# Kernel tuning notes

Measured on AMD Instinct MI355X. Metric: run time of the kernel, lower is better.

The kernel has to match this reference:

```python
import jax, jax.numpy as jnp
import numpy as np

# Grid constants from init_kwargs: output_shape = [1, 10, 200, 176, 64]
D, H, W, C = 10, 200, 176, 64
N_VOX = 30000


def _conv_block(x, w, scale, bias, stride, pad):
    # x: [N,C,D,H,W]; w: [O,I,kd,kh,kw]; ZeroPad3d then valid Conv3d,
    # then fused (inference) BatchNorm3d + ReLU.
    x = jnp.pad(x, ((0, 0), (0, 0), (pad[0], pad[0]), (pad[1], pad[1]), (pad[2], pad[2])))
    x = jax.lax.conv_general_dilated(
        x, w, window_strides=stride, padding='VALID',
        dimension_numbers=('NCDHW', 'OIDHW', 'NCDHW'))
    s = scale[None, :, None, None, None]
    b = bias[None, :, None, None, None]
    return jax.nn.relu(x * s + b)


def setup_inputs() -> dict:
    key = jax.random.key(0)
    kf, kd, kh, kw, k1, k2, k3, ks = jax.random.split(key, 8)
    voxel_features = jax.random.normal(kf, (N_VOX, C), dtype=jnp.float32)
    # coors columns: (batch_idx, d, h, w) each in range
    b_idx = jnp.zeros((N_VOX,), dtype=jnp.int32)  # batch_size = 1
    d_idx = jax.random.randint(kd, (N_VOX,), 0, D, dtype=jnp.int32)
    h_idx = jax.random.randint(kh, (N_VOX,), 0, H, dtype=jnp.int32)
    w_idx = jax.random.randint(kw, (N_VOX,), 0, W, dtype=jnp.int32)
    coors = jnp.stack([b_idx, d_idx, h_idx, w_idx], axis=1)
    fan = 1.0 / np.sqrt(C * 27)
    W1 = jax.random.normal(k1, (64, C, 3, 3, 3), dtype=jnp.float32) * fan
    W2 = jax.random.normal(k2, (64, 64, 3, 3, 3), dtype=jnp.float32) * fan
    W3 = jax.random.normal(k3, (64, 64, 3, 3, 3), dtype=jnp.float32) * fan
    ks1, ks2, ks3 = jax.random.split(ks, 3)
    scale1 = jax.random.uniform(ks1, (64,), dtype=jnp.float32, minval=0.5, maxval=1.5)
    scale2 = jax.random.uniform(ks2, (64,), dtype=jnp.float32, minval=0.5, maxval=1.5)
    scale3 = jax.random.uniform(ks3, (64,), dtype=jnp.float32, minval=0.5, maxval=1.5)
    bias1 = jax.random.normal(jax.random.fold_in(ks1, 1), (64,), dtype=jnp.float32) * 0.1
    bias2 = jax.random.normal(jax.random.fold_in(ks2, 1), (64,), dtype=jnp.float32) * 0.1
    bias3 = jax.random.normal(jax.random.fold_in(ks3, 1), (64,), dtype=jnp.float32) * 0.1
    return {
        'voxel_features': voxel_features, 'coors': coors, 'batch_size': 1,
        'W1': W1, 'scale1': scale1, 'bias1': bias1,
        'W2': W2, 'scale2': scale2, 'bias2': bias2,
        'W3': W3, 'scale3': scale3, 'bias3': bias3,
    }


def reference(voxel_features, coors, batch_size,
              W1, scale1, bias1, W2, scale2, bias2, W3, scale3, bias3):
    # scatter_nd: sparse voxel features -> dense [B, D, H, W, C]
    dense = jnp.zeros((batch_size, D, H, W, C), dtype=voxel_features.dtype)
    dense = dense.at[coors[:, 0], coors[:, 1], coors[:, 2], coors[:, 3]].set(voxel_features)
    x = dense.transpose(0, 4, 1, 2, 3)  # [B, C, D, H, W]
    # middle_conv: Pad(1)+Conv3d s=(2,1,1); Pad(0,1,1)+Conv3d s=1; Pad(1)+Conv3d s=(2,1,1)
    x = _conv_block(x, W1, scale1, bias1, (2, 1, 1), (1, 1, 1))   # D: 10 -> 5
    x = _conv_block(x, W2, scale2, bias2, (1, 1, 1), (0, 1, 1))   # D: 5 -> 3
    x = _conv_block(x, W3, scale3, bias3, (2, 1, 1), (1, 1, 1))   # D: 3 -> 2
    N, Cc, Dd, Hh, Ww = x.shape
    return x.reshape(N, Cc * Dd, Hh, Ww)  # [B, 128, H, W]
```

## Files before the change

### kernel.cpp

```cpp
#include <hip/hip_runtime.h>
#include <cstddef>

#define HH 200
#define WW 176
#define HP 202
#define WP 178
#define D_IN 10
#define D1 5
#define D2 3
#define D3 2
#define SLICE ((size_t)HP * WP * 64)

#define LA_SZ 51200
#define LB0   102400
#define LB_SZ 24576
#define LDS_TOTAL 151552

typedef _Float16 h8 __attribute__((ext_vector_type(8)));
typedef float f4 __attribute__((ext_vector_type(4)));

__device__ __forceinline__ void gl_lds16(const void* g, void* l) {
    __builtin_amdgcn_global_load_lds(
        (const __attribute__((address_space(1))) void*)g,
        (__attribute__((address_space(3))) void*)l, 16, 0, 0);
}

__global__ __launch_bounds__(256) void prep_k(const float* __restrict__ W1,
                                              const float* __restrict__ W2,
                                              const float* __restrict__ W3,
                                              _Float16* __restrict__ wdst,
                                              _Float16* __restrict__ A2,
                                              _Float16* __restrict__ A3,
                                              const int* __restrict__ coors,
                                              int* __restrict__ winner, int nvox) {
    const int b = blockIdx.x;
    if (b < 8) {
        _Float16* base = (b < D1) ? (A2 + (size_t)b * SLICE) : (A3 + (size_t)(b - D1) * SLICE);
        const h8 z = {};
        for (int t = threadIdx.x; t < 6080; t += 256) {
            size_t off;
            if (t < 2848) {
                int r = t / 1424, c = t - r * 1424;
                off = (size_t)(r ? (HP - 1) : 0) * WP * 64 + (size_t)c * 8;
            } else {
                int u = t - 2848;
                int c = u / 1616, v = u - c * 1616;
                int hr = v >> 3, o = v & 7;
                off = ((size_t)hr * WP + (c ? (WP - 1) : 0)) * 64 + (size_t)o * 8;
            }
            *(h8*)(base + off) = z;
        }
    } else if (b < 8 + 1296) {
        int idx = (b - 8) * 256 + threadIdx.x;
        if (idx < 3 * 27 * 64 * 64) {
            int set = idx / 110592;
            int r = idx - set * 110592;
            const float* src = set == 0 ? W1 : (set == 1 ? W2 : W3);
            int ci = r & 63;
            int co = (r >> 6) & 63;
            int tap = r >> 12;
            int s = ci >> 3, j = ci & 7;
            wdst[set * 110592 + tap * 4096 + co * 64 + (((s ^ (co & 7)) << 3) | j)] =
                (_Float16)src[(co * 64 + ci) * 27 + tap];
        }
    } else {
        int v = (b - 1304) * 256 + threadIdx.x;
        if (v < nvox) {
            int d = coors[v * 4 + 1], h = coors[v * 4 + 2], w = coors[v * 4 + 3];
            atomicMax(&winner[(d * HH + h) * WW + w], v + 1);
        }
    }
}

__global__ __launch_bounds__(256) void scatter_k(const float* __restrict__ feat,
                                                 const int* __restrict__ coors,
                                                 const int* __restrict__ winner,
                                                 _Float16* __restrict__ A, int nvox) {
    int v = blockIdx.x * 4 + (threadIdx.x >> 6);
    int ci = threadIdx.x & 63;
    if (v >= nvox) return;
    int d = coors[v * 4 + 1], h = coors[v * 4 + 2], w = coors[v * 4 + 3];
    if (winner[(d * HH + h) * WW + w] != v + 1) return;
    int P = w + 1;
    int swz = (((ci >> 3) ^ (P & 7)) << 3) | (ci & 7);
    A[(size_t)d * SLICE + ((size_t)(h + 1) * WP + P) * 64 + swz] = (_Float16)feat[v * 64 + ci];
}

template <int FINAL>
__global__ __launch_bounds__(512, 2) void conv_mfma_k(
    const _Float16* __restrict__ in, void* __restrict__ outp,
    const _Float16* __restrict__ wt,
    const float* __restrict__ scale, const float* __restrict__ bias,
    int inD, int strideD, int padD) {
    extern __shared__ char smem[];

    const int lane = threadIdx.x & 63;
    const int wave = threadIdx.x >> 6;
    const int l16 = lane & 15;
    const int quad = lane >> 4;
    const int h0 = blockIdx.y * 8;
    const int wb = blockIdx.x * 48;
    const int d = blockIdx.z;

    int kd_lo = padD - d * strideD; if (kd_lo < 0) kd_lo = 0;
    int kd_hi = inD - 1 - d * strideD + padD; if (kd_hi > 2) kd_hi = 2;
    const int P = 3 * (kd_hi - kd_lo + 1);

    auto stage = [&](int p, int par) {
        const int kd = kd_lo + p / 3;
        const int kh = p - 3 * (p / 3);
        const int zd = d * strideD + kd - padD;
        const _Float16* __restrict__ ap = in + (size_t)zd * SLICE;
        char* la = smem + par * LA_SZ;
        for (int j = wave; j < 50; j += 8) {
            int c = j * 64 + lane;
            int r = c / 400;
            int rem = c - r * 400;
            int px = rem >> 3, s = rem & 7;
            int g = wb + px; if (g > 177) g = 177;
            gl_lds16(ap + ((size_t)(h0 + kh + r) * WP + g) * 64 + s * 8, la + j * 1024);
        }
        const _Float16* __restrict__ wp = wt + (size_t)(kd * 9 + kh * 3) * 4096;
        char* lb = smem + LB0 + par * LB_SZ;
        for (int j = wave; j < 24; j += 8)
            gl_lds16(wp + (j * 64 + lane) * 8, lb + j * 1024);
    };

    f4 acc[3][4];
#pragma unroll
    for (int mt = 0; mt < 3; ++mt)
#pragma unroll
        for (int nt = 0; nt < 4; ++nt) acc[mt][nt] = (f4){0.f, 0.f, 0.f, 0.f};

    stage(0, 0);
    __syncthreads();

    for (int p = 0; p < P; ++p) {
        if (p + 1 < P) stage(p + 1, (p + 1) & 1);
        const _Float16* la = (const _Float16*)(smem + (p & 1) * LA_SZ);
        const _Float16* lb = (const _Float16*)(smem + LB0 + (p & 1) * LB_SZ);
#pragma unroll
        for (int kw = 0; kw < 3; ++kw) {
#pragma unroll
            for (int ch = 0; ch < 2; ++ch) {
                const int q = ch * 4 + quad;
                h8 b[4];
#pragma unroll
                for (int nt = 0; nt < 4; ++nt)
                    b[nt] = *(const h8*)(lb + (kw * 64 + nt * 16 + l16) * 64 +
                                         ((q ^ (l16 & 7)) << 3));
#pragma unroll
                for (int mt = 0; mt < 3; ++mt) {
                    const int px = mt * 16 + l16 + kw;
                    h8 a = *(const h8*)(la + (wave * 50 + px) * 64 + ((q ^ (px & 7)) << 3));
#pragma unroll
                    for (int nt = 0; nt < 4; ++nt)
                        acc[mt][nt] = __builtin_amdgcn_mfma_f32_16x16x32_f16(
                            a, b[nt], acc[mt][nt], 0, 0, 0);
                }
            }
        }
        __syncthreads();
    }

    const int h = h0 + wave;
#pragma unroll
    for (int nt = 0; nt < 4; ++nt) {
        const int co = nt * 16 + l16;
        const float s = scale[co];
        const float bb = bias[co];
#pragma unroll
        for (int mt = 0; mt < 3; ++mt) {
            const int w0 = wb + mt * 16 + quad * 4;
            if (w0 < WW) {
                if (FINAL) {
                    f4 v;
#pragma unroll
                    for (int r = 0; r < 4; ++r) {
                        float x = acc[mt][nt][r] * s + bb;
                        v[r] = x > 0.f ? x : 0.f;
                    }
                    *(f4*)((float*)outp + (((size_t)(co * 2 + d)) * HH + h) * WW + w0) = v;
                } else {
#pragma unroll
                    for (int r = 0; r < 4; ++r) {
                        float x = acc[mt][nt][r] * s + bb;
                        x = x > 0.f ? x : 0.f;
                        const int Pw = w0 + r + 1;
                        const int swz = (((co >> 3) ^ (Pw & 7)) << 3) | (co & 7);
                        ((_Float16*)outp)[(size_t)d * SLICE +
                            ((size_t)(h + 1) * WP + Pw) * 64 + swz] = (_Float16)x;
                    }
                }
            }
        }
    }
}

extern "C" void kernel_launch(void* const* d_in, const int* in_sizes, int n_in,
                              void* d_out, int out_size, void* d_ws, size_t ws_size,
                              hipStream_t stream) {
    const float* feat   = (const float*)d_in[0];
    const int*   coors  = (const int*)d_in[1];
    const float* W1     = (const float*)d_in[3];
    const float* scale1 = (const float*)d_in[4];
    const float* bias1  = (const float*)d_in[5];
    const float* W2     = (const float*)d_in[6];
    const float* scale2 = (const float*)d_in[7];
    const float* bias2  = (const float*)d_in[8];
    const float* W3     = (const float*)d_in[9];
    const float* scale3 = (const float*)d_in[10];
    const float* bias3  = (const float*)d_in[11];
    const int nvox = in_sizes[0] / 64;

    const size_t nA1 = (size_t)D_IN * SLICE;
    const size_t nWin = (size_t)D_IN * HH * WW;
    const size_t nA2 = (size_t)D1 * SLICE;
    const size_t nA3 = (size_t)D2 * SLICE;
    const size_t nWT = (size_t)27 * 64 * 64;

    _Float16* A1 = (_Float16*)d_ws;
    int* win = (int*)(A1 + nA1);
    _Float16* A2 = (_Float16*)(win + nWin);
    _Float16* A3 = A2 + nA2;
    _Float16* wt1 = A3 + nA3;
    _Float16* wt2 = wt1 + nWT;
    _Float16* wt3 = wt2 + nWT;

    hipFuncSetAttribute((const void*)conv_mfma_k<0>,
                        hipFuncAttributeMaxDynamicSharedMemorySize, LDS_TOTAL);
    hipFuncSetAttribute((const void*)conv_mfma_k<1>,
                        hipFuncAttributeMaxDynamicSharedMemorySize, LDS_TOTAL);

    hipMemsetAsync(d_ws, 0, nA1 * sizeof(_Float16) + nWin * sizeof(int), stream);

    const int win_blk = (nvox + 255) / 256;
    prep_k<<<8 + 1296 + win_blk, 256, 0, stream>>>(W1, W2, W3, wt1, A2, A3,
                                                   coors, win, nvox);
    scatter_k<<<(nvox + 3) / 4, 256, 0, stream>>>(feat, coors, win, A1, nvox);

    dim3 blk(512);
    conv_mfma_k<0><<<dim3(4, 25, D1), blk, LDS_TOTAL, stream>>>(A1, A2, wt1, scale1, bias1, D_IN, 2, 1);
    conv_mfma_k<0><<<dim3(4, 25, D2), blk, LDS_TOTAL, stream>>>(A2, A3, wt2, scale2, bias2, D1, 1, 0);
    conv_mfma_k<1><<<dim3(4, 25, D3), blk, LDS_TOTAL, stream>>>(A3, (float*)d_out, wt3, scale3, bias3, D2, 2, 1);
}
```

Before: 209.8 us.

## Stage full input halo per depth tap, read weights from global into registers

Each depth tap now loads the block's whole 10-row input halo into static LDS once, replacing the per-(kd,kh) double-buffered input and weight staging. Each of 4 waves computes two output rows, so the accumulators double. Weights are read unswizzled straight from global/L2 into registers per kh instead of through LDS. This cuts redundant input loads and LDS footprint, but removes load/compute overlap, adds register pressure, and makes every wave fetch weights from global memory.

```diff
diff --git a/kernel.cpp b/kernel.cpp
--- a/kernel.cpp
+++ b/kernel.cpp
@@ -10,11 +10,6 @@
 #define D2 3
 #define D3 2
 #define SLICE ((size_t)HP * WP * 64)
-
-#define LA_SZ 51200
-#define LB0   102400
-#define LB_SZ 24576
-#define LDS_TOTAL 151552
 
 typedef _Float16 h8 __attribute__((ext_vector_type(8)));
 typedef float f4 __attribute__((ext_vector_type(4)));
@@ -59,8 +54,7 @@
             int ci = r & 63;
             int co = (r >> 6) & 63;
             int tap = r >> 12;
-            int s = ci >> 3, j = ci & 7;
-            wdst[set * 110592 + tap * 4096 + co * 64 + (((s ^ (co & 7)) << 3) | j)] =
+            wdst[set * 110592 + tap * 4096 + co * 64 + ci] =
                 (_Float16)src[(co * 64 + ci) * 27 + tap];
         }
     } else {
@@ -87,12 +81,13 @@
 }
 
 template <int FINAL>
-__global__ __launch_bounds__(512, 2) void conv_mfma_k(
+__global__ __launch_bounds__(256, 2) void conv_mfma_k(
     const _Float16* __restrict__ in, void* __restrict__ outp,
     const _Float16* __restrict__ wt,
     const float* __restrict__ scale, const float* __restrict__ bias,
     int inD, int strideD, int padD) {
-    extern __shared__ char smem[];
+    __shared__ char smem_raw[64512];
+    _Float16* la = (_Float16*)smem_raw;
 
     const int lane = threadIdx.x & 63;
     const int wave = threadIdx.x >> 6;
@@ -104,92 +99,97 @@
 
     int kd_lo = padD - d * strideD; if (kd_lo < 0) kd_lo = 0;
     int kd_hi = inD - 1 - d * strideD + padD; if (kd_hi > 2) kd_hi = 2;
-    const int P = 3 * (kd_hi - kd_lo + 1);
-
-    auto stage = [&](int p, int par) {
-        const int kd = kd_lo + p / 3;
-        const int kh = p - 3 * (p / 3);
+
+    f4 acc[6][4];
+#pragma unroll
+    for (int mt = 0; mt < 6; ++mt)
+#pragma unroll
+        for (int nt = 0; nt < 4; ++nt) acc[mt][nt] = (f4){0.f, 0.f, 0.f, 0.f};
+
+    for (int kd = kd_lo; kd <= kd_hi; ++kd) {
         const int zd = d * strideD + kd - padD;
-        const _Float16* __restrict__ ap = in + (size_t)zd * SLICE;
-        char* la = smem + par * LA_SZ;
-        for (int j = wave; j < 50; j += 8) {
+        const _Float16* __restrict__ aplane = in + (size_t)zd * SLICE;
+
+        __syncthreads();
+        for (int j = wave; j < 63; j += 4) {
             int c = j * 64 + lane;
+            if (c > 3999) c = 3999;
             int r = c / 400;
             int rem = c - r * 400;
             int px = rem >> 3, s = rem & 7;
             int g = wb + px; if (g > 177) g = 177;
-            gl_lds16(ap + ((size_t)(h0 + kh + r) * WP + g) * 64 + s * 8, la + j * 1024);
-        }
-        const _Float16* __restrict__ wp = wt + (size_t)(kd * 9 + kh * 3) * 4096;
-        char* lb = smem + LB0 + par * LB_SZ;
-        for (int j = wave; j < 24; j += 8)
-            gl_lds16(wp + (j * 64 + lane) * 8, lb + j * 1024);
-    };
-
-    f4 acc[3][4];
-#pragma unroll
-    for (int mt = 0; mt < 3; ++mt)
-#pragma unroll
-        for (int nt = 0; nt < 4; ++nt) acc[mt][nt] = (f4){0.f, 0.f, 0.f, 0.f};
-
-    stage(0, 0);
-    __syncthreads();
-
-    for (int p = 0; p < P; ++p) {
-        if (p + 1 < P) stage(p + 1, (p + 1) & 1);
-        const _Float16* la = (const _Float16*)(smem + (p & 1) * LA_SZ);
-        const _Float16* lb = (const _Float16*)(smem + LB0 + (p & 1) * LB_SZ);
-#pragma unroll
-        for (int kw = 0; kw < 3; ++kw) {
-#pragma unroll
-            for (int ch = 0; ch < 2; ++ch) {
-                const int q = ch * 4 + quad;
-                h8 b[4];
-#pragma unroll
-                for (int nt = 0; nt < 4; ++nt)
-                    b[nt] = *(const h8*)(lb + (kw * 64 + nt * 16 + l16) * 64 +
-                                         ((q ^ (l16 & 7)) << 3));
-#pragma unroll
-                for (int mt = 0; mt < 3; ++mt) {
-                    const int px = mt * 16 + l16 + kw;
-                    h8 a = *(const h8*)(la + (wave * 50 + px) * 64 + ((q ^ (px & 7)) << 3));
+            gl_lds16(aplane + ((size_t)(h0 + r) * WP + g) * 64 + s * 8,
+                     smem_raw + j * 1024);
+        }
+        __syncthreads();
+
+        const _Float16* __restrict__ wkd = wt + (size_t)kd * 9 * 4096;
+#pragma unroll
+        for (int kh = 0; kh < 3; ++kh) {
+            h8 breg[3][2][4];
+#pragma unroll
+            for (int kw = 0; kw < 3; ++kw)
+#pragma unroll
+                for (int ch = 0; ch < 2; ++ch) {
+                    const int q = ch * 4 + quad;
 #pragma unroll
                     for (int nt = 0; nt < 4; ++nt)
-                        acc[mt][nt] = __builtin_amdgcn_mfma_f32_16x16x32_f16(
-                            a, b[nt], acc[mt][nt], 0, 0, 0);
+                        breg[kw][ch][nt] = *(const h8*)(
+                            wkd + (kh * 3 + kw) * 4096 + (nt * 16 + l16) * 64 + q * 8);
                 }
-            }
-        }
-        __syncthreads();
+#pragma unroll
+            for (int kw = 0; kw < 3; ++kw)
+#pragma unroll
+                for (int ch = 0; ch < 2; ++ch) {
+                    const int q = ch * 4 + quad;
+#pragma unroll
+                    for (int row = 0; row < 2; ++row)
+#pragma unroll
+                        for (int g = 0; g < 3; ++g) {
+                            const int px = g * 16 + l16 + kw;
+                            h8 a = *(const h8*)(la +
+                                ((wave * 2 + row + kh) * 50 + px) * 64 +
+                                ((q ^ (px & 7)) << 3));
+#pragma unroll
+                            for (int nt = 0; nt < 4; ++nt)
+                                acc[row * 3 + g][nt] =
+                                    __builtin_amdgcn_mfma_f32_16x16x32_f16(
+                                        a, breg[kw][ch][nt], acc[row * 3 + g][nt], 0, 0, 0);
+                        }
+                }
+        }
     }
 
-    const int h = h0 + wave;
 #pragma unroll
     for (int nt = 0; nt < 4; ++nt) {
         const int co = nt * 16 + l16;
         const float s = scale[co];
         const float bb = bias[co];
 #pragma unroll
-        for (int mt = 0; mt < 3; ++mt) {
-            const int w0 = wb + mt * 16 + quad * 4;
-            if (w0 < WW) {
-                if (FINAL) {
-                    f4 v;
-#pragma unroll
-                    for (int r = 0; r < 4; ++r) {
-                        float x = acc[mt][nt][r] * s + bb;
-                        v[r] = x > 0.f ? x : 0.f;
-                    }
-                    *(f4*)((float*)outp + (((size_t)(co * 2 + d)) * HH + h) * WW + w0) = v;
-                } else {
-#pragma unroll
-                    for (int r = 0; r < 4; ++r) {
-                        float x = acc[mt][nt][r] * s + bb;
-                        x = x > 0.f ? x : 0.f;
-                        const int Pw = w0 + r + 1;
-                        const int swz = (((co >> 3) ^ (Pw & 7)) << 3) | (co & 7);
-                        ((_Float16*)outp)[(size_t)d * SLICE +
-                            ((size_t)(h + 1) * WP + Pw) * 64 + swz] = (_Float16)x;
+        for (int row = 0; row < 2; ++row) {
+            const int h = h0 + wave * 2 + row;
+#pragma unroll
+            for (int g = 0; g < 3; ++g) {
+                const int w0 = wb + g * 16 + quad * 4;
+                if (w0 < WW) {
+                    if (FINAL) {
+                        f4 v;
+#pragma unroll
+                        for (int r = 0; r < 4; ++r) {
+                            float x = acc[row * 3 + g][nt][r] * s + bb;
+                            v[r] = x > 0.f ? x : 0.f;
+                        }
+                        *(f4*)((float*)outp + (((size_t)(co * 2 + d)) * HH + h) * WW + w0) = v;
+                    } else {
+#pragma unroll
+                        for (int r = 0; r < 4; ++r) {
+                            float x = acc[row * 3 + g][nt][r] * s + bb;
+                            x = x > 0.f ? x : 0.f;
+                            const int P = w0 + r + 1;
+                            const int swz = (((co >> 3) ^ (P & 7)) << 3) | (co & 7);
+                            ((_Float16*)outp)[(size_t)d * SLICE +
+                                ((size_t)(h + 1) * WP + P) * 64 + swz] = (_Float16)x;
+                        }
                     }
                 }
             }
@@ -227,11 +227,6 @@
     _Float16* wt2 = wt1 + nWT;
     _Float16* wt3 = wt2 + nWT;
 
-    hipFuncSetAttribute((const void*)conv_mfma_k<0>,
-                        hipFuncAttributeMaxDynamicSharedMemorySize, LDS_TOTAL);
-    hipFuncSetAttribute((const void*)conv_mfma_k<1>,
-                        hipFuncAttributeMaxDynamicSharedMemorySize, LDS_TOTAL);
-
     hipMemsetAsync(d_ws, 0, nA1 * sizeof(_Float16) + nWin * sizeof(int), stream);
 
     const int win_blk = (nvox + 255) / 256;
@@ -239,8 +234,8 @@
                                                    coors, win, nvox);
     scatter_k<<<(nvox + 3) / 4, 256, 0, stream>>>(feat, coors, win, A1, nvox);
 
-    dim3 blk(512);
-    conv_mfma_k<0><<<dim3(4, 25, D1), blk, LDS_TOTAL, stream>>>(A1, A2, wt1, scale1, bias1, D_IN, 2, 1);
-    conv_mfma_k<0><<<dim3(4, 25, D2), blk, LDS_TOTAL, stream>>>(A2, A3, wt2, scale2, bias2, D1, 1, 0);
-    conv_mfma_k<1><<<dim3(4, 25, D3), blk, LDS_TOTAL, stream>>>(A3, (float*)d_out, wt3, scale3, bias3, D2, 2, 1);
-}
+    dim3 blk(256);
+    conv_mfma_k<0><<<dim3(4, 25, D1), blk, 0, stream>>>(A1, A2, wt1, scale1, bias1, D_IN, 2, 1);
+    conv_mfma_k<0><<<dim3(4, 25, D2), blk, 0, stream>>>(A2, A3, wt2, scale2, bias2, D1, 1, 0);
+    conv_mfma_k<1><<<dim3(4, 25, D3), blk, 0, stream>>>(A3, (float*)d_out, wt3, scale3, bias3, D2, 2, 1);
+}
```

New measurement: 309.1 us. 47.3% more time.
